# Optimization experiments

Measured on AMD Instinct MI355X. Metric: run time of the kernel, lower is better.

Reference implementation:

```python
import jax, jax.numpy as jnp
import numpy as np

EMBED = 512
HEADS = 64
DK = EMBED // HEADS  # == n_wires_attn == 8
NW_FFN = 8
FFN = 2048
EPS = 1e-5


def _layernorm(x, g, b):
    mu = jnp.mean(x, axis=-1, keepdims=True)
    var = jnp.var(x, axis=-1, keepdims=True)
    return (x - mu) * jax.lax.rsqrt(var + EPS) * g + b


def setup_inputs() -> dict:
    key = jax.random.key(0)
    ks = jax.random.split(key, 12)
    d = {
        "x": jax.random.normal(ks[0], (4, 1024, EMBED), dtype=jnp.float32),
        # attention quantum RX params (one per wire, shared across heads/tokens)
        "phi": jax.random.normal(ks[1], (DK,), dtype=jnp.float32) * 0.1,
        # combine_heads linear
        "Wc": jax.random.normal(ks[2], (EMBED, EMBED), dtype=jnp.float32) / np.sqrt(EMBED),
        "bc": jnp.zeros((EMBED,), dtype=jnp.float32),
        # FFN quantum RY params
        "theta": jax.random.normal(ks[3], (NW_FFN,), dtype=jnp.float32) * 0.1,
        "W1": jax.random.normal(ks[4], (NW_FFN, FFN), dtype=jnp.float32) / np.sqrt(NW_FFN),
        "b1": jnp.zeros((FFN,), dtype=jnp.float32),
        "W2": jax.random.normal(ks[5], (FFN, EMBED), dtype=jnp.float32) / np.sqrt(FFN),
        "b2": jnp.zeros((EMBED,), dtype=jnp.float32),
        "g1": jnp.ones((EMBED,), dtype=jnp.float32),
        "be1": jnp.zeros((EMBED,), dtype=jnp.float32),
        "g2": jnp.ones((EMBED,), dtype=jnp.float32),
        "be2": jnp.zeros((EMBED,), dtype=jnp.float32),
    }
    return d


def reference(x, phi, Wc, bc, theta, W1, b1, W2, b2, g1, be1, g2, be2):
    B, S, E = x.shape
    # --- quantum attention projections ---
    # Per head-row of DK features: RX(x_i) encoder then trainable RX(phi_i),
    xh = x.reshape(B, S, HEADS, DK)
    qkv = jnp.cos(xh + phi)                     # [B,S,H,DK]
    qkv = jnp.transpose(qkv, (0, 2, 1, 3))      # [B,H,S,DK]
    scores = jnp.einsum('bhqd,bhkd->bhqk', qkv, qkv) / jnp.sqrt(jnp.float32(DK))
    attn = jax.nn.softmax(scores, axis=-1)
    out = jnp.einsum('bhqk,bhkd->bhqd', attn, qkv)
    out = jnp.transpose(out, (0, 2, 1, 3)).reshape(B, S, E)
    attn_out = out @ Wc.T if False else out @ Wc + bc  # combine_heads linear
    x1 = _layernorm(x + attn_out, g1, be1)
    # --- quantum FFN: RX(x_i) then trainable RY(theta_i) -> <Z> = cos(x_i)*cos(theta_i)
    qout = jnp.cos(x1[..., :NW_FFN]) * jnp.cos(theta)   # [B,S,NW_FFN]
    h = jax.nn.relu(qout @ W1 + b1)
    ffn_out = h @ W2 + b2
    return _layernorm(x1 + ffn_out, g2, be2)
```

## Files before the change

### kernel.cpp

```cpp
#include <hip/hip_runtime.h>
#include <hip/hip_bf16.h>
#include <math.h>

#define B 4
#define S 1024
#define E 512
#define H 64
#define DK 8
#define FFN 2048
#define BS (B*S)

#define CSCALE 0.7141879f

#if __has_builtin(__builtin_amdgcn_exp2f)
#define EXP2F(x) __builtin_amdgcn_exp2f(x)
#else
#define EXP2F(x) exp2f(x)
#endif

typedef __attribute__((ext_vector_type(8))) short short8;
typedef __attribute__((ext_vector_type(4))) float float4a;

union U8 { short8 v; unsigned u[4]; };
union F4 { float4a v; float f[4]; };

__device__ __forceinline__ unsigned short f2bf(float f) {
    unsigned u = __builtin_bit_cast(unsigned, f);
    u = (u + 0x7fffu + ((u >> 16) & 1u)) >> 16;
    return (unsigned short)u;
}
__device__ __forceinline__ float bf2f(unsigned short h) {
    return __builtin_bit_cast(float, (unsigned)h << 16);
}
__device__ __forceinline__ unsigned packbf(float a, float b) {
    return __builtin_amdgcn_perm(__builtin_bit_cast(unsigned, a),
                                 __builtin_bit_cast(unsigned, b), 0x07060302u);
}
__device__ __forceinline__ unsigned packbf_rn(float a, float b) {
    return ((unsigned)f2bf(a) << 16) | f2bf(b);
}
__device__ __forceinline__ int pidx(int k) {
    return (k & ~31) | (((k >> 2) & 3) << 3) | (((k >> 4) & 1) << 2) | (k & 3);
}

__global__ __launch_bounds__(256) void convert_kernel(const float* __restrict__ Wc,
                                                      const float* __restrict__ W2,
                                                      const float* __restrict__ W1,
                                                      const float* __restrict__ b1,
                                                      unsigned short* __restrict__ W2f,
                                                      unsigned short* __restrict__ Wcf,
                                                      unsigned short* __restrict__ W1f) {
    int idx = blockIdx.x * 256 + threadIdx.x;
    if (idx < 131072) {
        int lane = idx & 63, c = idx >> 6;
        int ntile = c >> 6, kb32 = c & 63;
        int g = lane >> 4, col = lane & 15;
        int n = ntile * 16 + col, kb = kb32 * 32;
        short8 o;
        #pragma unroll
        for (int j = 0; j < 8; j++) {
            int k = kb + 16 * (j >> 2) + 4 * g + (j & 3);
            o[j] = (short)f2bf(W2[(size_t)k * 512 + n]);
        }
        *(short8*)&W2f[(size_t)idx * 8] = o;
    } else if (idx < 163840) {
        int i2 = idx - 131072;
        int lane = i2 & 63, c = i2 >> 6;
        int ntile = c >> 4, kb32 = c & 15;
        int g = lane >> 4, col = lane & 15;
        int n = ntile * 16 + col, kb = kb32 * 32;
        short8 o;
        #pragma unroll
        for (int j = 0; j < 8; j++)
            o[j] = (short)f2bf(Wc[(size_t)(kb + g * 8 + j) * 512 + n]);
        *(short8*)&Wcf[(size_t)i2 * 8] = o;
    } else {
        int i3 = idx - 163840;
        int lane = i3 & 63, c = i3 >> 6;
        int g = lane >> 4, col = lane & 15;
        int f = (c >> 1) * 32 + (c & 1) * 16 + col;
        short8 o = {0,0,0,0,0,0,0,0};
        if (g == 0) {
            #pragma unroll
            for (int j = 0; j < 8; j++) o[j] = (short)f2bf(W1[j * FFN + f]);
        } else if (g == 1) {
            o[0] = (short)f2bf(b1[f]);
        }
        *(short8*)&W1f[(size_t)i3 * 8] = o;
    }
}

__global__ __launch_bounds__(256) void attn_mfma_kernel(const float* __restrict__ x,
                                                        const float* __restrict__ phi,
                                                        unsigned short* __restrict__ Afrag) {
    int head = blockIdx.x >> 2, qquad = blockIdx.x & 3;
    int b = head >> 6, hh = head & 63;

    __shared__ unsigned short kv[S * DK];
    __shared__ unsigned short vtp[9][S + 8];

    float ph[DK];
    #pragma unroll
    for (int d = 0; d < DK; d++) ph[d] = phi[d];

    int tid = threadIdx.x;
    for (int r = tid; r < S; r += 256) {
        const float* xp = x + ((size_t)(b * S + r)) * E + hh * DK;
        float4 u = *(const float4*)xp;
        float4 v = *(const float4*)(xp + 4);
        float c[8] = {__cosf(u.x+ph[0]), __cosf(u.y+ph[1]), __cosf(u.z+ph[2]), __cosf(u.w+ph[3]),
                      __cosf(v.x+ph[4]), __cosf(v.y+ph[5]), __cosf(v.z+ph[6]), __cosf(v.w+ph[7])};
        unsigned* kp = (unsigned*)&kv[r * DK];
        #pragma unroll
        for (int d = 0; d < 4; d++)
            kp[d] = packbf_rn(c[2*d+1] * CSCALE, c[2*d] * CSCALE);
        int pr = pidx(r);
        #pragma unroll
        for (int d = 0; d < DK; d++) vtp[d][pr] = f2bf(c[d]);
        vtp[8][pr] = 0x3F80;
    }
    __syncthreads();

    int w = tid >> 6, lane = tid & 63, col = lane & 15, g = lane >> 4;
    bool g0 = (g == 0);
    int q0 = qquad * 256 + w * 64;
    const short8 z8 = {0,0,0,0,0,0,0,0};
    const float4a zc = {0.f,0.f,0.f,0.f};

    short8 aq[4];
    #pragma unroll
    for (int t = 0; t < 4; t++)
        aq[t] = g0 ? *(const short8*)&kv[(q0 + t*16 + col) * DK] : z8;

    float4a acc[4];
    #pragma unroll
    for (int t = 0; t < 4; t++) acc[t] = zc;

    int vrow = col < 8 ? col : 8;
    const unsigned short* vbase = &vtp[vrow][0];

    for (int kb = 0; kb < S; kb += 32) {
        short8 bk0 = g0 ? *(const short8*)&kv[(kb + col) * DK] : z8;
        short8 bk1 = g0 ? *(const short8*)&kv[(kb + 16 + col) * DK] : z8;
        short8 vf = *(const short8*)(vbase + kb + g * 8);
        #pragma unroll
        for (int t = 0; t < 4; t++) {
            float4a s0 = __builtin_amdgcn_mfma_f32_16x16x32_bf16(bk0, aq[t], zc, 0,0,0);
            float4a s1 = __builtin_amdgcn_mfma_f32_16x16x32_bf16(bk1, aq[t], zc, 0,0,0);
            F4 S0, S1; S0.v = s0; S1.v = s1;
            float e00 = EXP2F(S0.f[0]);
            float e01 = EXP2F(S0.f[1]);
            float e02 = EXP2F(S0.f[2]);
            float e03 = EXP2F(S0.f[3]);
            float e10 = EXP2F(S1.f[0]);
            float e11 = EXP2F(S1.f[1]);
            float e12 = EXP2F(S1.f[2]);
            float e13 = EXP2F(S1.f[3]);
            U8 pf;
            pf.u[0] = packbf(e01, e00);
            pf.u[1] = packbf(e03, e02);
            pf.u[2] = packbf(e11, e10);
            pf.u[3] = packbf(e13, e12);
            acc[t] = __builtin_amdgcn_mfma_f32_16x16x32_bf16(vf, pf.v, acc[t], 0,0,0);
        }
    }
    int lp8 = ((hh & 3) * 16 + col) * 8;
    #pragma unroll
    for (int t = 0; t < 4; t++) {
        F4 a; a.v = acc[t];
        float denom = __shfl(a.f[0], 32 + col);
        float inv = __builtin_amdgcn_rcpf(denom);
        if (g < 2) {
            int chunk = (hh >> 2) * 256 + ((b << 6) | (qquad << 4) | (w << 2) | t);
            uint2 o;
            o.x = packbf_rn(a.f[1] * inv, a.f[0] * inv);
            o.y = packbf_rn(a.f[3] * inv, a.f[2] * inv);
            *(uint2*)&Afrag[(size_t)chunk * 512 + lp8 + g * 4] = o;
        }
    }
}

__global__ __launch_bounds__(256) void combine_mfma(const unsigned short* __restrict__ Afrag,
                                                    const unsigned short* __restrict__ Wcf,
                                                    const float* __restrict__ bias,
                                                    unsigned short* __restrict__ Cbf) {
    int tid = threadIdx.x;
    int w = tid >> 6, lane = tid & 63;
    int col = lane & 15, g = lane >> 4;
    int ttile = blockIdx.x * 4 + w;
    int nt0 = blockIdx.y * 4;
    const float4a zc = {0.f,0.f,0.f,0.f};

    float4a acc[4];
    #pragma unroll
    for (int nt = 0; nt < 4; nt++) acc[nt] = zc;

    for (int kb32 = 0; kb32 < 16; kb32++) {
        short8 af = *(const short8*)&Afrag[((size_t)(kb32 * 256 + ttile) * 64 + lane) * 8];
        #pragma unroll
        for (int nt = 0; nt < 4; nt++) {
            short8 bf = *(const short8*)&Wcf[((size_t)((nt0 + nt) * 16 + kb32) * 64 + lane) * 8];
            acc[nt] = __builtin_amdgcn_mfma_f32_16x16x32_bf16(af, bf, acc[nt], 0, 0, 0);
        }
    }
    int crow = ttile * 16 + g * 4;
    #pragma unroll
    for (int nt = 0; nt < 4; nt++) {
        int n = nt0 * 16 + nt * 16 + col;
        float bb = bias[n];
        #pragma unroll
        for (int r = 0; r < 4; r++)
            Cbf[(size_t)(crow + r) * 512 + n] = f2bf(acc[nt][r] + bb);
    }
}

__global__ __launch_bounds__(256) void ffn_mfma(const unsigned short* __restrict__ qbf,
                                                const unsigned short* __restrict__ W1fg,
                                                const unsigned short* __restrict__ W2f,
                                                const float* __restrict__ b2,
                                                unsigned short* __restrict__ Cbf) {
    __shared__ unsigned short w1x[FFN * 16];
    int tid = threadIdx.x;
    #pragma unroll
    for (int i = 0; i < 16; i++) {
        int d = tid + i * 256;
        int f = d >> 1, gg = d & 1;
        int kb32 = f >> 5, half = (f >> 4) & 1, fc = f & 15;
        int src = ((kb32 * 2 + half) * 64 + gg * 16 + fc);
        *(short8*)&w1x[f * 16 + gg * 8] = *(const short8*)&W1fg[(size_t)src * 8];
    }
    __syncthreads();

    int w = tid >> 6, lane = tid & 63, col = lane & 15, g = lane >> 4;
    int mw = blockIdx.x * 128 + w * 32;
    int ntile0 = blockIdx.y * 2;
    const short8 z8 = {0,0,0,0,0,0,0,0};
    const short8 one8 = {(short)0x3F80,0,0,0,0,0,0,0};
    const float4a zc = {0.f,0.f,0.f,0.f};

    short8 qf[2];
    #pragma unroll
    for (int t = 0; t < 2; t++)
        qf[t] = (g == 0) ? *(const short8*)&qbf[(size_t)(mw + t * 16 + col) * 8]
                         : (g == 1 ? one8 : z8);

    float4a acc[2][2];
    acc[0][0] = zc; acc[0][1] = zc; acc[1][0] = zc; acc[1][1] = zc;

    const unsigned short* w2p0 = W2f + (size_t)(ntile0 * 64) * 512 + lane * 8;
    const unsigned short* w2p1 = W2f + (size_t)((ntile0 + 1) * 64) * 512 + lane * 8;

    for (int kb32 = 0; kb32 < 64; kb32++) {
        int kb = kb32 * 32;
        short8 w1f0 = (g < 2) ? *(const short8*)&w1x[(kb + col) * 16 + g * 8] : z8;
        short8 w1f1 = (g < 2) ? *(const short8*)&w1x[(kb + 16 + col) * 16 + g * 8] : z8;
        short8 af0 = *(const short8*)(w2p0 + (size_t)kb32 * 512);
        short8 af1 = *(const short8*)(w2p1 + (size_t)kb32 * 512);
        #pragma unroll
        for (int t = 0; t < 2; t++) {
            float4a h0 = __builtin_amdgcn_mfma_f32_16x16x32_bf16(w1f0, qf[t], zc, 0,0,0);
            float4a h1 = __builtin_amdgcn_mfma_f32_16x16x32_bf16(w1f1, qf[t], zc, 0,0,0);
            F4 H0, H1; H0.v = h0; H1.v = h1;
            float e00 = fmaxf(H0.f[0], 0.f);
            float e01 = fmaxf(H0.f[1], 0.f);
            float e02 = fmaxf(H0.f[2], 0.f);
            float e03 = fmaxf(H0.f[3], 0.f);
            float e10 = fmaxf(H1.f[0], 0.f);
            float e11 = fmaxf(H1.f[1], 0.f);
            float e12 = fmaxf(H1.f[2], 0.f);
            float e13 = fmaxf(H1.f[3], 0.f);
            U8 pf;
            pf.u[0] = packbf(e01, e00);
            pf.u[1] = packbf(e03, e02);
            pf.u[2] = packbf(e11, e10);
            pf.u[3] = packbf(e13, e12);
            acc[t][0] = __builtin_amdgcn_mfma_f32_16x16x32_bf16(af0, pf.v, acc[t][0], 0,0,0);
            acc[t][1] = __builtin_amdgcn_mfma_f32_16x16x32_bf16(af1, pf.v, acc[t][1], 0,0,0);
        }
    }
    int n0 = ntile0 * 16;
    #pragma unroll
    for (int nt = 0; nt < 2; nt++) {
        float4 bb = *(const float4*)&b2[n0 + nt * 16 + 4 * g];
        #pragma unroll
        for (int t = 0; t < 2; t++) {
            F4 a; a.v = acc[t][nt];
            uint2 o;
            o.x = packbf_rn(a.f[1] + bb.y, a.f[0] + bb.x);
            o.y = packbf_rn(a.f[3] + bb.w, a.f[2] + bb.z);
            *(uint2*)&Cbf[(size_t)(mw + t * 16 + col) * 512 + n0 + nt * 16 + 4 * g] = o;
        }
    }
}

__global__ __launch_bounds__(256) void ln_kernel(const float* a,
                                                 const unsigned short* __restrict__ r,
                                                 const float* __restrict__ g,
                                                 const float* __restrict__ be,
                                                 float* out,
                                                 unsigned short* __restrict__ qoutbf,
                                                 const float* __restrict__ theta) {
    int t = blockIdx.x, tid = threadIdx.x;
    size_t base = (size_t)t * E;
    int e0 = tid * 2;
    float2 av = *(const float2*)&a[base + e0];
    unsigned rv = *(const unsigned*)&r[base + e0];
    float v0 = av.x + bf2f((unsigned short)(rv & 0xffff));
    float v1 = av.y + bf2f((unsigned short)(rv >> 16));
    float s  = v0 + v1;
    float sq = v0 * v0 + v1 * v1;
    #pragma unroll
    for (int off = 32; off > 0; off >>= 1) {
        s  += __shfl_down(s, off);
        sq += __shfl_down(sq, off);
    }
    __shared__ float ls[4], lq[4];
    int wave = tid >> 6, lane = tid & 63;
    if (lane == 0) { ls[wave] = s; lq[wave] = sq; }
    __syncthreads();
    if (tid == 0) {
        float SS = ls[0] + ls[1] + ls[2] + ls[3];
        float QQ = lq[0] + lq[1] + lq[2] + lq[3];
        float mu = SS * (1.f / E);
        float var = QQ * (1.f / E) - mu * mu;
        ls[0] = mu;
        lq[0] = rsqrtf(var + 1e-5f);
    }
    __syncthreads();
    float mu = ls[0], rstd = lq[0];
    float2 gv = *(const float2*)&g[e0];
    float2 bv = *(const float2*)&be[e0];
    float y0 = (v0 - mu) * rstd * gv.x + bv.x;
    float y1 = (v1 - mu) * rstd * gv.y + bv.y;
    *(float2*)&out[base + e0] = make_float2(y0, y1);
    if (qoutbf != nullptr && tid < 4) {
        float q0v = __cosf(y0) * __cosf(theta[e0]);
        float q1v = __cosf(y1) * __cosf(theta[e0 + 1]);
        *(unsigned*)&qoutbf[t * DK + e0] = packbf_rn(q1v, q0v);
    }
}

extern "C" void kernel_launch(void* const* d_in, const int* in_sizes, int n_in,
                              void* d_out, int out_size, void* d_ws, size_t ws_size,
                              hipStream_t stream) {
    const float* x     = (const float*)d_in[0];
    const float* phi   = (const float*)d_in[1];
    const float* Wc    = (const float*)d_in[2];
    const float* bc    = (const float*)d_in[3];
    const float* theta = (const float*)d_in[4];
    const float* W1    = (const float*)d_in[5];
    const float* b1    = (const float*)d_in[6];
    const float* W2    = (const float*)d_in[7];
    const float* b2    = (const float*)d_in[8];
    const float* g1    = (const float*)d_in[9];
    const float* be1   = (const float*)d_in[10];
    const float* g2    = (const float*)d_in[11];
    const float* be2   = (const float*)d_in[12];
    float* out = (float*)d_out;

    float* ws = (float*)d_ws;
    unsigned short* proj   = (unsigned short*)ws;
    unsigned short* W2f    = (unsigned short*)(ws + 1048576);
    unsigned short* Wcf    = (unsigned short*)(ws + 1572864);
    unsigned short* W1f    = (unsigned short*)(ws + 1703936);
    unsigned short* qoutbf = (unsigned short*)(ws + 1736704);
    unsigned short* Afrag  = (unsigned short*)d_out;

    convert_kernel<<<672, 256, 0, stream>>>(Wc, W2, W1, b1, W2f, Wcf, W1f);
    attn_mfma_kernel<<<B * H * 4, 256, 0, stream>>>(x, phi, Afrag);
    combine_mfma<<<dim3(64, 8), 256, 0, stream>>>(Afrag, Wcf, bc, proj);
    ln_kernel<<<BS, 256, 0, stream>>>(x, proj, g1, be1, out, qoutbf, theta);
    ffn_mfma<<<dim3(32, 16), 256, 0, stream>>>(qoutbf, W1f, W2f, b2, proj);
    ln_kernel<<<BS, 256, 0, stream>>>(out, proj, g2, be2, out, nullptr, nullptr);
}
```

Before: 193.6 us.

## Fuse weight conversion into attention, merge combine GEMM with first LayerNorm

Merges the weight-conversion kernel into the attention kernel as extra blocks, and switches attention blocks to 512 threads covering half the queries each. Replaces the branching key-fragment loads with an offset into a zero-padded LDS row. Fuses the combine-heads GEMM with the first LayerNorm and the quantum FFN feature computation, so the bf16 projection round trip and one launch disappear. Also doubles the FFN block size. The fused kernels cut launches and global traffic, but each GEMM now runs on fewer, larger blocks.

```diff
diff --git a/kernel.cpp b/kernel.cpp
--- a/kernel.cpp
+++ b/kernel.cpp
@@ -43,68 +43,72 @@
     return (k & ~31) | (((k >> 2) & 3) << 3) | (((k >> 4) & 1) << 2) | (k & 3);
 }
 
-__global__ __launch_bounds__(256) void convert_kernel(const float* __restrict__ Wc,
-                                                      const float* __restrict__ W2,
-                                                      const float* __restrict__ W1,
-                                                      const float* __restrict__ b1,
-                                                      unsigned short* __restrict__ W2f,
-                                                      unsigned short* __restrict__ Wcf,
-                                                      unsigned short* __restrict__ W1f) {
-    int idx = blockIdx.x * 256 + threadIdx.x;
-    if (idx < 131072) {
-        int lane = idx & 63, c = idx >> 6;
-        int ntile = c >> 6, kb32 = c & 63;
-        int g = lane >> 4, col = lane & 15;
-        int n = ntile * 16 + col, kb = kb32 * 32;
-        short8 o;
-        #pragma unroll
-        for (int j = 0; j < 8; j++) {
-            int k = kb + 16 * (j >> 2) + 4 * g + (j & 3);
-            o[j] = (short)f2bf(W2[(size_t)k * 512 + n]);
-        }
-        *(short8*)&W2f[(size_t)idx * 8] = o;
-    } else if (idx < 163840) {
-        int i2 = idx - 131072;
-        int lane = i2 & 63, c = i2 >> 6;
-        int ntile = c >> 4, kb32 = c & 15;
-        int g = lane >> 4, col = lane & 15;
-        int n = ntile * 16 + col, kb = kb32 * 32;
-        short8 o;
-        #pragma unroll
-        for (int j = 0; j < 8; j++)
-            o[j] = (short)f2bf(Wc[(size_t)(kb + g * 8 + j) * 512 + n]);
-        *(short8*)&Wcf[(size_t)i2 * 8] = o;
-    } else {
-        int i3 = idx - 163840;
-        int lane = i3 & 63, c = i3 >> 6;
-        int g = lane >> 4, col = lane & 15;
-        int f = (c >> 1) * 32 + (c & 1) * 16 + col;
-        short8 o = {0,0,0,0,0,0,0,0};
-        if (g == 0) {
+__global__ __launch_bounds__(512) void attn_conv_kernel(const float* __restrict__ x,
+                                                        const float* __restrict__ phi,
+                                                        const float* __restrict__ Wc,
+                                                        const float* __restrict__ W2,
+                                                        const float* __restrict__ W1,
+                                                        const float* __restrict__ b1,
+                                                        unsigned short* __restrict__ Afrag,
+                                                        unsigned short* __restrict__ W2f,
+                                                        unsigned short* __restrict__ Wcf,
+                                                        unsigned short* __restrict__ W1f) {
+    __shared__ unsigned short kv[(S + 16) * DK];
+    __shared__ unsigned short vtp[9][S + 8];
+    int bid = blockIdx.x;
+    int tid = threadIdx.x;
+
+    if (bid >= 512) {
+        int idx = (bid - 512) * 512 + tid;
+        if (idx < 131072) {
+            int lane = idx & 63, c = idx >> 6;
+            int ntile = c >> 6, kb32 = c & 63;
+            int g = lane >> 4, col = lane & 15;
+            int n = ntile * 16 + col, kb = kb32 * 32;
+            short8 o;
             #pragma unroll
-            for (int j = 0; j < 8; j++) o[j] = (short)f2bf(W1[j * FFN + f]);
-        } else if (g == 1) {
-            o[0] = (short)f2bf(b1[f]);
-        }
-        *(short8*)&W1f[(size_t)i3 * 8] = o;
-    }
-}
-
-__global__ __launch_bounds__(256) void attn_mfma_kernel(const float* __restrict__ x,
-                                                        const float* __restrict__ phi,
-                                                        unsigned short* __restrict__ Afrag) {
-    int head = blockIdx.x >> 2, qquad = blockIdx.x & 3;
+            for (int j = 0; j < 8; j++) {
+                int k = kb + 16 * (j >> 2) + 4 * g + (j & 3);
+                o[j] = (short)f2bf(W2[(size_t)k * 512 + n]);
+            }
+            *(short8*)&W2f[(size_t)idx * 8] = o;
+        } else if (idx < 163840) {
+            int i2 = idx - 131072;
+            int lane = i2 & 63, c = i2 >> 6;
+            int ntile = c >> 4, kb32 = c & 15;
+            int g = lane >> 4, col = lane & 15;
+            int n = ntile * 16 + col, kb = kb32 * 32;
+            short8 o;
+            #pragma unroll
+            for (int j = 0; j < 8; j++)
+                o[j] = (short)f2bf(Wc[(size_t)(kb + g * 8 + j) * 512 + n]);
+            *(short8*)&Wcf[(size_t)i2 * 8] = o;
+        } else {
+            int i3 = idx - 163840;
+            int lane = i3 & 63, c = i3 >> 6;
+            int g = lane >> 4, col = lane & 15;
+            int f = (c >> 1) * 32 + (c & 1) * 16 + col;
+            short8 o = {0,0,0,0,0,0,0,0};
+            if (g == 0) {
+                #pragma unroll
+                for (int j = 0; j < 8; j++) o[j] = (short)f2bf(W1[j * FFN + f]);
+            } else if (g == 1) {
+                o[0] = (short)f2bf(b1[f]);
+            }
+            *(short8*)&W1f[(size_t)i3 * 8] = o;
+        }
+        return;
+    }
+
+    int head = bid >> 1, qhalf = bid & 1;
     int b = head >> 6, hh = head & 63;
 
-    __shared__ unsigned short kv[S * DK];
-    __shared__ unsigned short vtp[9][S + 8];
-
     float ph[DK];
     #pragma unroll
     for (int d = 0; d < DK; d++) ph[d] = phi[d];
 
-    int tid = threadIdx.x;
-    for (int r = tid; r < S; r += 256) {
+    const short8 z8 = {0,0,0,0,0,0,0,0};
+    for (int r = tid; r < S; r += 512) {
         const float* xp = x + ((size_t)(b * S + r)) * E + hh * DK;
         float4 u = *(const float4*)xp;
         float4 v = *(const float4*)(xp + 4);
@@ -119,12 +123,12 @@
         for (int d = 0; d < DK; d++) vtp[d][pr] = f2bf(c[d]);
         vtp[8][pr] = 0x3F80;
     }
+    if (tid < 16) *(short8*)&kv[(S + tid) * DK] = z8;
     __syncthreads();
 
     int w = tid >> 6, lane = tid & 63, col = lane & 15, g = lane >> 4;
     bool g0 = (g == 0);
-    int q0 = qquad * 256 + w * 64;
-    const short8 z8 = {0,0,0,0,0,0,0,0};
+    int q0 = qhalf * 512 + w * 64;
     const float4a zc = {0.f,0.f,0.f,0.f};
 
     short8 aq[4];
@@ -139,9 +143,14 @@
     int vrow = col < 8 ? col : 8;
     const unsigned short* vbase = &vtp[vrow][0];
 
+    int off0 = g0 ? col * DK : S * DK;
+    int off1 = g0 ? (16 + col) * DK : S * DK;
+    int stepo = g0 ? 32 * DK : 0;
+
     for (int kb = 0; kb < S; kb += 32) {
-        short8 bk0 = g0 ? *(const short8*)&kv[(kb + col) * DK] : z8;
-        short8 bk1 = g0 ? *(const short8*)&kv[(kb + 16 + col) * DK] : z8;
+        short8 bk0 = *(const short8*)&kv[off0];
+        short8 bk1 = *(const short8*)&kv[off1];
+        off0 += stepo; off1 += stepo;
         short8 vf = *(const short8*)(vbase + kb + g * 8);
         #pragma unroll
         for (int t = 0; t < 4; t++) {
@@ -171,7 +180,7 @@
         float denom = __shfl(a.f[0], 32 + col);
         float inv = __builtin_amdgcn_rcpf(denom);
         if (g < 2) {
-            int chunk = (hh >> 2) * 256 + ((b << 6) | (qquad << 4) | (w << 2) | t);
+            int chunk = (hh >> 2) * 256 + ((b << 6) | (qhalf << 5) | (w << 2) | t);
             uint2 o;
             o.x = packbf_rn(a.f[1] * inv, a.f[0] * inv);
             o.y = packbf_rn(a.f[3] * inv, a.f[2] * inv);
@@ -180,41 +189,95 @@
     }
 }
 
-__global__ __launch_bounds__(256) void combine_mfma(const unsigned short* __restrict__ Afrag,
-                                                    const unsigned short* __restrict__ Wcf,
-                                                    const float* __restrict__ bias,
-                                                    unsigned short* __restrict__ Cbf) {
+__global__ __launch_bounds__(512) void combine_ln1(const unsigned short* __restrict__ Afrag,
+                                                   const unsigned short* __restrict__ Wcf,
+                                                   const float* __restrict__ bc,
+                                                   const float* __restrict__ x,
+                                                   const float* __restrict__ g1,
+                                                   const float* __restrict__ be1,
+                                                   float* __restrict__ x1out,
+                                                   unsigned short* __restrict__ qoutbf,
+                                                   const float* __restrict__ theta) {
+    __shared__ unsigned short As[16 * 64 * 8];
+    __shared__ float xout[16][516];
+    int tt = blockIdx.x;
     int tid = threadIdx.x;
-    int w = tid >> 6, lane = tid & 63;
-    int col = lane & 15, g = lane >> 4;
-    int ttile = blockIdx.x * 4 + w;
-    int nt0 = blockIdx.y * 4;
+
+    for (int i = tid; i < 1024; i += 512)
+        *(short8*)&As[i * 8] =
+            *(const short8*)&Afrag[((size_t)((i >> 6) * 256 + tt) * 64 + (i & 63)) * 8];
+    __syncthreads();
+
+    int w = tid >> 6, lane = tid & 63, col = lane & 15, g = lane >> 4;
     const float4a zc = {0.f,0.f,0.f,0.f};
-
     float4a acc[4];
     #pragma unroll
     for (int nt = 0; nt < 4; nt++) acc[nt] = zc;
 
     for (int kb32 = 0; kb32 < 16; kb32++) {
-        short8 af = *(const short8*)&Afrag[((size_t)(kb32 * 256 + ttile) * 64 + lane) * 8];
+        short8 af = *(const short8*)&As[(kb32 * 64 + lane) * 8];
         #pragma unroll
         for (int nt = 0; nt < 4; nt++) {
-            short8 bf = *(const short8*)&Wcf[((size_t)((nt0 + nt) * 16 + kb32) * 64 + lane) * 8];
+            short8 bf = *(const short8*)&Wcf[((size_t)((w * 4 + nt) * 16 + kb32) * 64 + lane) * 8];
             acc[nt] = __builtin_amdgcn_mfma_f32_16x16x32_bf16(af, bf, acc[nt], 0, 0, 0);
         }
     }
-    int crow = ttile * 16 + g * 4;
     #pragma unroll
     for (int nt = 0; nt < 4; nt++) {
-        int n = nt0 * 16 + nt * 16 + col;
-        float bb = bias[n];
+        int n = w * 64 + nt * 16 + col;
+        float bb = bc[n];
         #pragma unroll
         for (int r = 0; r < 4; r++)
-            Cbf[(size_t)(crow + r) * 512 + n] = f2bf(acc[nt][r] + bb);
-    }
-}
-
-__global__ __launch_bounds__(256) void ffn_mfma(const unsigned short* __restrict__ qbf,
+            xout[g * 4 + r][n] = acc[nt][r] + bb;
+    }
+    __syncthreads();
+
+    int hl = lane >> 5, l = lane & 31;
+    int token = w * 2 + hl;
+    int e0 = l * 16;
+    size_t grow = ((size_t)tt * 16 + token) * 512;
+    float v[16];
+    float s = 0.f, sq = 0.f;
+    #pragma unroll
+    for (int u = 0; u < 4; u++) {
+        float4 xv = *(const float4*)&x[grow + e0 + u * 4];
+        float4 pv = *(const float4*)&xout[token][e0 + u * 4];
+        float a0 = xv.x + pv.x, a1 = xv.y + pv.y, a2 = xv.z + pv.z, a3 = xv.w + pv.w;
+        v[u*4] = a0; v[u*4+1] = a1; v[u*4+2] = a2; v[u*4+3] = a3;
+        s += a0 + a1 + a2 + a3;
+        sq += a0*a0 + a1*a1 + a2*a2 + a3*a3;
+    }
+    #pragma unroll
+    for (int off = 1; off <= 16; off <<= 1) {
+        s  += __shfl_xor(s, off);
+        sq += __shfl_xor(sq, off);
+    }
+    float mu = s * (1.f / 512.f);
+    float var = sq * (1.f / 512.f) - mu * mu;
+    float rstd = rsqrtf(var + 1e-5f);
+    float y[16];
+    #pragma unroll
+    for (int u = 0; u < 4; u++) {
+        float4 gv = *(const float4*)&g1[e0 + u * 4];
+        float4 bv = *(const float4*)&be1[e0 + u * 4];
+        y[u*4]   = (v[u*4]   - mu) * rstd * gv.x + bv.x;
+        y[u*4+1] = (v[u*4+1] - mu) * rstd * gv.y + bv.y;
+        y[u*4+2] = (v[u*4+2] - mu) * rstd * gv.z + bv.z;
+        y[u*4+3] = (v[u*4+3] - mu) * rstd * gv.w + bv.w;
+        float4 o = make_float4(y[u*4], y[u*4+1], y[u*4+2], y[u*4+3]);
+        *(float4*)&x1out[grow + e0 + u * 4] = o;
+    }
+    if (l == 0) {
+        U8 q;
+        q.u[0] = packbf_rn(__cosf(y[1]) * __cosf(theta[1]), __cosf(y[0]) * __cosf(theta[0]));
+        q.u[1] = packbf_rn(__cosf(y[3]) * __cosf(theta[3]), __cosf(y[2]) * __cosf(theta[2]));
+        q.u[2] = packbf_rn(__cosf(y[5]) * __cosf(theta[5]), __cosf(y[4]) * __cosf(theta[4]));
+        q.u[3] = packbf_rn(__cosf(y[7]) * __cosf(theta[7]), __cosf(y[6]) * __cosf(theta[6]));
+        *(short8*)&qoutbf[((size_t)tt * 16 + token) * 8] = q.v;
+    }
+}
+
+__global__ __launch_bounds__(512) void ffn_mfma(const unsigned short* __restrict__ qbf,
                                                 const unsigned short* __restrict__ W1fg,
                                                 const unsigned short* __restrict__ W2f,
                                                 const float* __restrict__ b2,
@@ -222,8 +285,8 @@
     __shared__ unsigned short w1x[FFN * 16];
     int tid = threadIdx.x;
     #pragma unroll
-    for (int i = 0; i < 16; i++) {
-        int d = tid + i * 256;
+    for (int i = 0; i < 8; i++) {
+        int d = tid + i * 512;
         int f = d >> 1, gg = d & 1;
         int kb32 = f >> 5, half = (f >> 4) & 1, fc = f & 15;
         int src = ((kb32 * 2 + half) * 64 + gg * 16 + fc);
@@ -232,7 +295,7 @@
     __syncthreads();
 
     int w = tid >> 6, lane = tid & 63, col = lane & 15, g = lane >> 4;
-    int mw = blockIdx.x * 128 + w * 32;
+    int mw = blockIdx.x * 256 + w * 32;
     int ntile0 = blockIdx.y * 2;
     const short8 z8 = {0,0,0,0,0,0,0,0};
     const short8 one8 = {(short)0x3F80,0,0,0,0,0,0,0};
@@ -297,9 +360,7 @@
                                                  const unsigned short* __restrict__ r,
                                                  const float* __restrict__ g,
                                                  const float* __restrict__ be,
-                                                 float* out,
-                                                 unsigned short* __restrict__ qoutbf,
-                                                 const float* __restrict__ theta) {
+                                                 float* out) {
     int t = blockIdx.x, tid = threadIdx.x;
     size_t base = (size_t)t * E;
     int e0 = tid * 2;
@@ -333,11 +394,6 @@
     float y0 = (v0 - mu) * rstd * gv.x + bv.x;
     float y1 = (v1 - mu) * rstd * gv.y + bv.y;
     *(float2*)&out[base + e0] = make_float2(y0, y1);
-    if (qoutbf != nullptr && tid < 4) {
-        float q0v = __cosf(y0) * __cosf(theta[e0]);
-        float q1v = __cosf(y1) * __cosf(theta[e0 + 1]);
-        *(unsigned*)&qoutbf[t * DK + e0] = packbf_rn(q1v, q0v);
-    }
 }
 
 extern "C" void kernel_launch(void* const* d_in, const int* in_sizes, int n_in,
@@ -359,17 +415,16 @@
     float* out = (float*)d_out;
 
     float* ws = (float*)d_ws;
-    unsigned short* proj   = (unsigned short*)ws;
+    unsigned short* Afrag  = (unsigned short*)ws;
     unsigned short* W2f    = (unsigned short*)(ws + 1048576);
     unsigned short* Wcf    = (unsigned short*)(ws + 1572864);
     unsigned short* W1f    = (unsigned short*)(ws + 1703936);
     unsigned short* qoutbf = (unsigned short*)(ws + 1736704);
-    unsigned short* Afrag  = (unsigned short*)d_out;
-
-    convert_kernel<<<672, 256, 0, stream>>>(Wc, W2, W1, b1, W2f, Wcf, W1f);
-    attn_mfma_kernel<<<B * H * 4, 256, 0, stream>>>(x, phi, Afrag);
-    combine_mfma<<<dim3(64, 8), 256, 0, stream>>>(Afrag, Wcf, bc, proj);
-    ln_kernel<<<BS, 256, 0, stream>>>(x, proj, g1, be1, out, qoutbf, theta);
-    ffn_mfma<<<dim3(32, 16), 256, 0, stream>>>(qoutbf, W1f, W2f, b2, proj);
-    ln_kernel<<<BS, 256, 0, stream>>>(out, proj, g2, be2, out, nullptr, nullptr);
-}
+
+    attn_conv_kernel<<<848, 512, 0, stream>>>(x, phi, Wc, W2, W1, b1,
+                                              Afrag, W2f, Wcf, W1f);
+    combine_ln1<<<256, 512, 0, stream>>>(Afrag, Wcf, bc, x, g1, be1,
+                                         out, qoutbf, theta);
+    ffn_mfma<<<dim3(16, 16), 512, 0, stream>>>(qoutbf, W1f, W2f, b2, Afrag);
+    ln_kernel<<<BS, 256, 0, stream>>>(out, Afrag, g2, be2, out);
+}
```

Measured after the change: 164.8 us. 1.18x faster.
